# Optimization experiments

Measured on AMD Instinct MI355X. Metric: run time of the kernel, lower is better.

The kernel has to match this reference:

```python
import jax, jax.numpy as jnp
import numpy as np

B, N, D, H = 2, 2048, 2048, 16
HD = D // H  # head_dim = 128


def _rope(x, cos, sin):
    # x: [B,H,N,HD]; cos/sin: [N,HD]. use_real=True, use_real_unbind_dim=-1 (interleaved pairs).
    xr = x[..., 0::2]
    xi = x[..., 1::2]
    x_rot = jnp.stack([-xi, xr], axis=-1).reshape(x.shape)
    return x * cos[None, None] + x_rot * sin[None, None]


def setup_inputs() -> dict:
    key = jax.random.key(0)
    ks = jax.random.split(key, 10)
    x = jax.random.normal(ks[0], (B, N, D), dtype=jnp.float32)
    # realistic RoPE tables
    inv_freq = 1.0 / (10000.0 ** (np.arange(0, HD, 2, dtype=np.float32) / HD))
    t = np.arange(N, dtype=np.float32)
    ang = np.einsum('n,f->nf', t, inv_freq)           # [N, HD/2]
    ang = np.repeat(ang, 2, axis=-1)                  # [N, HD] interleaved
    cos = jnp.asarray(np.cos(ang))
    sin = jnp.asarray(np.sin(ang))
    s = 0.02
    Wq = jax.random.normal(ks[1], (D, D), dtype=jnp.float32) * s
    Wk = jax.random.normal(ks[2], (D, D), dtype=jnp.float32) * s
    Wv = jax.random.normal(ks[3], (D, D), dtype=jnp.float32) * s
    Wo = jax.random.normal(ks[4], (D, D), dtype=jnp.float32) * s
    bq = jnp.zeros((D,), jnp.float32)
    bk = jnp.zeros((D,), jnp.float32)
    bv = jnp.zeros((D,), jnp.float32)
    bo = jnp.zeros((D,), jnp.float32)
    return {"x": x, "cos": cos, "sin": sin, "Wq": Wq, "bq": bq, "Wk": Wk,
            "bk": bk, "Wv": Wv, "bv": bv, "Wo": Wo, "bo": bo}


def reference(x, cos, sin, Wq, bq, Wk, bk, Wv, bv, Wo, bo):
    scale = HD ** -0.5
    q = x @ Wq + bq
    k = x @ Wk + bk
    v = x @ Wv + bv
    # b n (h c) -> b h n c
    def split_heads(t):
        return t.reshape(B, N, H, HD).transpose(0, 2, 1, 3)
    q, k, v = split_heads(q), split_heads(k), split_heads(v)
    q = q * scale  # module's dp_scale
    q = _rope(q, cos, sin)
    k = _rope(k, cos, sin)
    # flash_attn_func(softmax_scale=None) applies head_dim^-0.5 AGAIN -> effective HD^-1
    logits = jnp.einsum('bhqc,bhkc->bhqk', q, k) * scale
    attn = jax.nn.softmax(logits, axis=-1)
    o = jnp.einsum('bhqk,bhkc->bhqc', attn, v)
    o = o.transpose(0, 2, 1, 3).reshape(B, N, D)  # b h n c -> b n (h c)
    return o @ Wo + bo
```

## Files before the change

### kernel.cpp

```cpp
#include <hip/hip_runtime.h>

typedef unsigned short u16;
typedef unsigned int u32;
typedef __attribute__((ext_vector_type(8))) short bfx8;
typedef __attribute__((ext_vector_type(4))) float fx4;
typedef __attribute__((ext_vector_type(16))) float fx16;
typedef __attribute__((ext_vector_type(4))) unsigned short u16x4;

#define MFMA_BF16(a,b,c)   __builtin_amdgcn_mfma_f32_16x16x32_bf16((a),(b),(c),0,0,0)
#define MFMA32_BF16(a,b,c) __builtin_amdgcn_mfma_f32_32x32x16_bf16((a),(b),(c),0,0,0)

#define BATCH 2
#define SEQ   2048
#define DM    2048
#define NH    16
#define HD    128
#define MR    4096

__device__ __forceinline__ u16 f2bf(float f){
  union{float f; unsigned u;} v; v.f = f;
  unsigned r = v.u + 0x7FFFu + ((v.u >> 16) & 1u);
  return (u16)(r >> 16);
}
__device__ __forceinline__ unsigned cvtpk(float lo, float hi){
  unsigned r;
  asm("v_cvt_pk_bf16_f32 %0, %1, %2" : "=v"(r) : "v"(lo), "v"(hi));
  return r;
}
__device__ __forceinline__ void gll16(const void* g, void* l){
  __builtin_amdgcn_global_load_lds(
      (const __attribute__((address_space(1))) void*)g,
      (__attribute__((address_space(3))) void*)l, 16, 0, 0);
}

__global__ __launch_bounds__(256) void k_cast(const float* __restrict__ in,
                                              u16* __restrict__ o, int n4){
  int gid = blockIdx.x*256 + threadIdx.x;
  if (gid >= n4) return;
  float4 x = ((const float4*)in)[gid];
  u16x4 v = {f2bf(x.x), f2bf(x.y), f2bf(x.z), f2bf(x.w)};
  ((u16x4*)o)[gid] = v;
}

__global__ __launch_bounds__(256) void k_twcat(const float* __restrict__ Wq,
                                               const float* __restrict__ Wk,
                                               const float* __restrict__ Wv,
                                               u16* __restrict__ Th){
  __shared__ float T[64][65];
  int z = blockIdx.z;
  const float* W = (z==0) ? Wq : (z==1) ? Wk : Wv;
  int n0 = blockIdx.x*64, k0 = blockIdx.y*64;
  int t = threadIdx.x;
  int r = t>>2, c = (t&3)*16;
  const float* src = W + (size_t)(k0+r)*DM + n0 + c;
  #pragma unroll
  for (int j=0;j<4;j++){
    float4 v = *(const float4*)(src + 4*j);
    T[r][c+4*j+0]=v.x; T[r][c+4*j+1]=v.y; T[r][c+4*j+2]=v.z; T[r][c+4*j+3]=v.w;
  }
  __syncthreads();
  int nr = t>>2, kc = (t&3)*16;
  size_t ob = (size_t)(z*DM + n0+nr)*DM + k0 + kc;
  #pragma unroll
  for (int j=0;j<16;j+=4){
    u16x4 vh;
    #pragma unroll
    for (int q=0;q<4;q++) vh[q] = f2bf(T[kc+j+q][nr]);
    *(u16x4*)(Th+ob+j)=vh;
  }
}

__global__ __launch_bounds__(256) void k_tw(const float* __restrict__ W, u16* __restrict__ Th){
  __shared__ float T[64][65];
  int n0 = blockIdx.x*64, k0 = blockIdx.y*64;
  int t = threadIdx.x;
  int r = t>>2, c = (t&3)*16;
  const float* src = W + (size_t)(k0+r)*DM + n0 + c;
  #pragma unroll
  for (int j=0;j<4;j++){
    float4 v = *(const float4*)(src + 4*j);
    T[r][c+4*j+0]=v.x; T[r][c+4*j+1]=v.y; T[r][c+4*j+2]=v.z; T[r][c+4*j+3]=v.w;
  }
  __syncthreads();
  int nr = t>>2, kc = (t&3)*16;
  size_t ob = (size_t)(n0+nr)*DM + k0 + kc;
  #pragma unroll
  for (int j=0;j<16;j+=4){
    u16x4 vh;
    #pragma unroll
    for (int q=0;q<4;q++) vh[q] = f2bf(T[kc+j+q][nr]);
    *(u16x4*)(Th+ob+j)=vh;
  }
}

__global__ __launch_bounds__(256) void k_gemm_qkv(
    const u16* __restrict__ A, const u16* __restrict__ B,
    const float* __restrict__ bqp, const float* __restrict__ bkp, const float* __restrict__ bvp,
    const float* __restrict__ cs, const float* __restrict__ sn,
    u16* __restrict__ qb, u16* __restrict__ kb, u16* __restrict__ vt)
{
  __shared__ u16 sA[128*64], sB[128*64];
  const int K = DM;
  const int tid = threadIdx.x;
  const int lane = tid & 63;
  const int w = tid >> 6;
  const int g = lane >> 4, qi = lane & 15;
  const int wr = w >> 1, wc = w & 1;
  const int bm = blockIdx.y * 128;
  const int bn = blockIdx.x * 128;

  int r_[4], sc_[4];
  #pragma unroll
  for (int i=0;i<4;i++){
    int off = w*4096 + i*1024 + lane*16;
    int r = off>>7, cb = off&127;
    r_[i] = r; sc_[i] = (cb ^ ((r&7)<<4)) >> 1;
  }

  fx4 acc[4][4] = {};

  for (int k0 = 0; k0 < K; k0 += 64){
    __syncthreads();
    #pragma unroll
    for (int i=0;i<4;i++){
      gll16(A + (size_t)(bm + r_[i])*K + k0 + sc_[i], &sA[w*2048 + i*512]);
      gll16(B + (size_t)(bn + r_[i])*K + k0 + sc_[i], &sB[w*2048 + i*512]);
    }
    __syncthreads();

    #pragma unroll
    for (int kk=0;kk<2;kk++){
      const int cb = kk*64 + g*16;
      bfx8 fa[4], fb[4];
      #pragma unroll
      for (int m=0;m<4;m++){
        int row = wr*64 + m*16 + qi;
        fa[m] = *(const bfx8*)((const char*)sA + row*128 + (cb ^ ((row&7)<<4)));
      }
      #pragma unroll
      for (int n=0;n<4;n++){
        int row = wc*64 + n*16 + qi;
        fb[n] = *(const bfx8*)((const char*)sB + row*128 + (cb ^ ((row&7)<<4)));
      }
      #pragma unroll
      for (int m=0;m<4;m++)
        #pragma unroll
        for (int n=0;n<4;n++)
          acc[m][n] = MFMA_BF16(fa[m], fb[n], acc[m][n]);
    }
  }

  const int sec = bn >> 11;
  if (sec < 2){
    u16* dst = sec ? kb : qb;
    const float* bias = sec ? bkp : bqp;
    const float qs = sec ? 1.0f : (1.4426950408889634f/128.0f);
    #pragma unroll
    for (int m=0;m<4;m++){
      #pragma unroll
      for (int n=0;n<4;n++){
        int col = bn + wc*64 + n*16 + qi;
        int cq = col & 2047, hh = cq>>7, d = cq&127;
        float bc = bias[cq];
        float sgn = (d&1) ? 1.0f : -1.0f;
        #pragma unroll
        for (int r=0;r<4;r++){
          int row = bm + wr*64 + m*16 + g*4 + r;
          int bI = row>>11, nr2 = row&2047;
          float v = (acc[m][n][r] + bc)*qs;
          float p = __shfl_xor(v, 1, 64);
          float c = cs[nr2*HD + d], s = sn[nr2*HD + d];
          float y = v*c + sgn*p*s;
          dst[((size_t)(bI*NH+hh)*SEQ + nr2)*HD + d] = f2bf(y);
        }
      }
    }
  } else {
    #pragma unroll
    for (int m=0;m<4;m++){
      #pragma unroll
      for (int n=0;n<4;n++){
        int col = bn + wc*64 + n*16 + qi;
        int cv = col & 2047, hh = cv>>7, d = cv&127;
        float bc = bvp[cv];
        int row0 = bm + wr*64 + m*16 + g*4;
        int bI = row0>>11, n0_ = row0&2047;
        u16x4 pk;
        #pragma unroll
        for (int r=0;r<4;r++) pk[r] = f2bf(acc[m][n][r] + bc);
        *(u16x4*)(vt + ((size_t)(bI*NH+hh)*HD + d)*SEQ + n0_) = pk;
      }
    }
  }
}

__global__ __launch_bounds__(256) void k_gemm(
    const u16* __restrict__ A, const u16* __restrict__ B,
    const float* __restrict__ bias, float* __restrict__ C,
    int M, int N, int K)
{
  __shared__ u16 sA[128*64], sB[128*64];
  const int tid = threadIdx.x;
  const int lane = tid & 63;
  const int w = tid >> 6;
  const int g = lane >> 4, qi = lane & 15;
  const int wr = w >> 1, wc = w & 1;
  const int bm = blockIdx.y * 128;
  const int bn = blockIdx.x * 128;

  int r_[4], sc_[4];
  #pragma unroll
  for (int i=0;i<4;i++){
    int off = w*4096 + i*1024 + lane*16;
    int r = off>>7, cb = off&127;
    r_[i] = r; sc_[i] = (cb ^ ((r&7)<<4)) >> 1;
  }

  fx4 acc[4][4] = {};

  for (int k0 = 0; k0 < K; k0 += 64){
    __syncthreads();
    #pragma unroll
    for (int i=0;i<4;i++){
      gll16(A + (size_t)(bm + r_[i])*K + k0 + sc_[i], &sA[w*2048 + i*512]);
      gll16(B + (size_t)(bn + r_[i])*K + k0 + sc_[i], &sB[w*2048 + i*512]);
    }
    __syncthreads();

    #pragma unroll
    for (int kk=0;kk<2;kk++){
      const int cb = kk*64 + g*16;
      bfx8 fa[4], fb[4];
      #pragma unroll
      for (int m=0;m<4;m++){
        int row = wr*64 + m*16 + qi;
        fa[m] = *(const bfx8*)((const char*)sA + row*128 + (cb ^ ((row&7)<<4)));
      }
      #pragma unroll
      for (int n=0;n<4;n++){
        int row = wc*64 + n*16 + qi;
        fb[n] = *(const bfx8*)((const char*)sB + row*128 + (cb ^ ((row&7)<<4)));
      }
      #pragma unroll
      for (int m=0;m<4;m++)
        #pragma unroll
        for (int n=0;n<4;n++)
          acc[m][n] = MFMA_BF16(fa[m], fb[n], acc[m][n]);
    }
  }

  #pragma unroll
  for (int m=0;m<4;m++){
    #pragma unroll
    for (int n=0;n<4;n++){
      int col = bn + wc*64 + n*16 + qi;
      float bc = bias[col];
      #pragma unroll
      for (int r=0;r<4;r++){
        int row = bm + wr*64 + m*16 + g*4 + r;
        C[(size_t)row*N + col] = acc[m][n][r] + bc;
      }
    }
  }
}

__global__ __launch_bounds__(128) void k_flash(const u16* __restrict__ Q, const u16* __restrict__ Kb,
                                               const u16* __restrict__ Vt, u16* __restrict__ O){
  __shared__ union SM {
    struct { u16 k[64*128]; u16 v[128*64]; } s;
    u16 ob[64*128];
  } sm;
  const int tid = threadIdx.x, lane = tid & 63, w = tid >> 6;
  const int bid = blockIdx.x;
  const int qt = bid & 31, h = (bid>>5)&15, b = bid>>9;
  const int bh = b*NH + h;
  const int qb0 = qt*64;
  const int hi = lane >> 5, qi = lane & 31;
  const u16* Kb2 = Kb + (size_t)bh*SEQ*HD;
  const u16* Vt2 = Vt + (size_t)bh*SEQ*HD;

  bfx8 qf[8];
  {
    const u16* qp = Q + ((size_t)bh*SEQ + qb0 + w*32 + qi)*HD + hi*8;
    #pragma unroll
    for (int ks=0; ks<8; ++ks) qf[ks] = *(const bfx8*)(qp + ks*16);
  }

  u32 koff[8], voff[8];
  #pragma unroll
  for (int i=0;i<8;i++){
    int off = w*8192 + i*1024 + lane*16;
    int kr = off>>8, kc = off&255;
    int kcs = kc ^ ((kr&15)<<4);
    koff[i] = kr*HD + (kcs>>1);
    int vr = off>>7, vc = off&127;
    int vcs = vc ^ ((vr&7)<<4);
    voff[i] = vr*SEQ + (vcs>>1);
  }

#define STAGE_K(kv_) do { _Pragma("unroll") \
    for (int i_=0;i_<8;i_++) gll16(Kb2 + koff[i_] + (u32)(kv_)*HD, &sm.s.k[w*4096 + i_*512]); } while(0)
#define STAGE_V(kv_) do { _Pragma("unroll") \
    for (int i_=0;i_<8;i_++) gll16(Vt2 + voff[i_] + (u32)(kv_),    &sm.s.v[w*4096 + i_*512]); } while(0)

  fx16 accO0 = {}, accO1 = {}, accO2 = {}, accO3 = {};
  float mrun = -1e30f, lrun = 0.f;

  STAGE_K(0);
  STAGE_V(0);

  for (int t=0; t<32; ++t){
    asm volatile("s_waitcnt vmcnt(8)" ::: "memory");
    __builtin_amdgcn_s_barrier();

    fx16 stA = {}, stB = {};
    __builtin_amdgcn_s_setprio(1);
    #pragma unroll
    for (int ks=0; ks<8; ++ks){
      const int cb = ks*32 + hi*16;
      int rowA = qi;
      int rowB = 32 + qi;
      bfx8 kfa = *(const bfx8*)((const char*)sm.s.k + rowA*256 + (cb ^ ((rowA&15)<<4)));
      bfx8 kfb = *(const bfx8*)((const char*)sm.s.k + rowB*256 + (cb ^ ((rowB&15)<<4)));
      stA = MFMA32_BF16(kfa, qf[ks], stA);
      stB = MFMA32_BF16(kfb, qf[ks], stB);
    }
    __builtin_amdgcn_s_setprio(0);
    __builtin_amdgcn_s_barrier();
    if (t < 31) STAGE_K(t*64 + 64);

    float pm = stA[0];
    #pragma unroll
    for (int i=1;i<16;i++) pm = fmaxf(pm, stA[i]);
    #pragma unroll
    for (int i=0;i<16;i++) pm = fmaxf(pm, stB[i]);
    pm = fmaxf(pm, __shfl_xor(pm, 32, 64));
    if (!__all(pm <= mrun + 11.0f)){
      float mn = fmaxf(mrun, pm);
      float al = exp2f(mrun - mn);
      lrun *= al;
      accO0 *= al; accO1 *= al; accO2 *= al; accO3 *= al;
      mrun = mn;
    }
    float ps = 0.f;
    #pragma unroll
    for (int i=0;i<16;i++){
      float p0 = exp2f(stA[i] - mrun); stA[i] = p0; ps += p0;
      float p1 = exp2f(stB[i] - mrun); stB[i] = p1; ps += p1;
    }
    lrun += ps;

    bfx8 pv0, pv1, pv2, pv3;
#define PACK(pvx_, stX_, base_) do { \
      unsigned a0 = cvtpk(stX_[base_+0], stX_[base_+1]); \
      unsigned a1 = cvtpk(stX_[base_+2], stX_[base_+3]); \
      unsigned b0 = cvtpk(stX_[base_+4], stX_[base_+5]); \
      unsigned b1 = cvtpk(stX_[base_+6], stX_[base_+7]); \
      asm volatile("v_permlane32_swap_b32 %0, %1" : "+v"(a0), "+v"(b0)); \
      asm volatile("v_permlane32_swap_b32 %0, %1" : "+v"(a1), "+v"(b1)); \
      union { bfx8 v; unsigned u[4]; } pu_; \
      pu_.u[0] = a0; pu_.u[1] = a1; pu_.u[2] = b0; pu_.u[3] = b1; \
      pvx_ = pu_.v; } while(0)
    PACK(pv0, stA, 0);
    PACK(pv1, stA, 8);
    PACK(pv2, stB, 0);
    PACK(pv3, stB, 8);
#undef PACK

    asm volatile("s_waitcnt vmcnt(8)" ::: "memory");
    if (t == 31) asm volatile("s_waitcnt vmcnt(0)" ::: "memory");
    __builtin_amdgcn_s_barrier();

    __builtin_amdgcn_s_setprio(1);
    #pragma unroll
    for (int dblk=0; dblk<4; ++dblk){
      const int row = dblk*32 + qi;
      const int swz = (row&7)<<4;
      const char* vrow = (const char*)sm.s.v + row*128;
      bfx8 vf0 = *(const bfx8*)(vrow + ((0*32 + hi*16) ^ swz));
      bfx8 vf1 = *(const bfx8*)(vrow + ((1*32 + hi*16) ^ swz));
      bfx8 vf2 = *(const bfx8*)(vrow + ((2*32 + hi*16) ^ swz));
      bfx8 vf3 = *(const bfx8*)(vrow + ((3*32 + hi*16) ^ swz));
      fx16 a = (dblk==0)?accO0:(dblk==1)?accO1:(dblk==2)?accO2:accO3;
      a = MFMA32_BF16(vf0, pv0, a);
      a = MFMA32_BF16(vf1, pv1, a);
      a = MFMA32_BF16(vf2, pv2, a);
      a = MFMA32_BF16(vf3, pv3, a);
      if (dblk==0) accO0 = a; else if (dblk==1) accO1 = a; else if (dblk==2) accO2 = a; else accO3 = a;
    }
    __builtin_amdgcn_s_setprio(0);
    __builtin_amdgcn_s_barrier();
    if (t < 31) STAGE_V(t*64 + 64);
  }
#undef STAGE_K
#undef STAGE_V

  {
    float l = lrun + __shfl_xor(lrun, 32, 64);
    float inv = 1.0f / l;
    int q = w*32 + qi;
    char* obr = (char*)sm.ob + q*256;
    const int swz = (q&7)<<4;
#define OWRITE(accX_, dblk_) do { _Pragma("unroll") \
    for (int p=0;p<8;p++){ \
      int d = dblk_*32 + 2*(p&1) + 8*(p>>1) + 4*hi; \
      unsigned wv = cvtpk(accX_[2*p]*inv, accX_[2*p+1]*inv); \
      *(unsigned*)(obr + ((d*2) ^ swz)) = wv; } } while(0)
    OWRITE(accO0, 0); OWRITE(accO1, 1); OWRITE(accO2, 2); OWRITE(accO3, 3);
#undef OWRITE
  }
  __syncthreads();
  {
    int q2 = tid>>1, c0 = (tid&1)*64;
    u16* dst = O + (size_t)(b*SEQ + qb0 + q2)*DM + h*HD + c0;
    #pragma unroll
    for (int jj=0;jj<8;jj++){
      int d0 = c0 + jj*8;
      bfx8 v = *(const bfx8*)((const char*)sm.ob + q2*256 + ((d0*2) ^ ((q2&7)<<4)));
      *(bfx8*)(dst + jj*8) = v;
    }
  }
}

extern "C" void kernel_launch(void* const* d_in, const int* in_sizes, int n_in,
                              void* d_out, int out_size, void* d_ws, size_t ws_size,
                              hipStream_t stream){
  (void)in_sizes; (void)n_in; (void)out_size; (void)ws_size;
  const float* x  = (const float*)d_in[0];
  const float* cs = (const float*)d_in[1];
  const float* sn = (const float*)d_in[2];
  const float* Wq = (const float*)d_in[3];
  const float* bq = (const float*)d_in[4];
  const float* Wk = (const float*)d_in[5];
  const float* bk = (const float*)d_in[6];
  const float* Wv = (const float*)d_in[7];
  const float* bv = (const float*)d_in[8];
  const float* Wo = (const float*)d_in[9];
  const float* bo = (const float*)d_in[10];
  float* out = (float*)d_out;

  char* ws = (char*)d_ws;
  const size_t MB = 1048576;
  u16* xb   = (u16*)(ws);
  u16* wt   = (u16*)(ws + 16*MB);
  u16* qb   = (u16*)(ws + 40*MB);
  u16* kb   = (u16*)(ws + 56*MB);
  u16* vt   = (u16*)(ws + 72*MB);
  u16* ob16 = (u16*)(ws + 88*MB);

  k_cast<<<8192,256,0,stream>>>(x, xb, 2097152);
  k_twcat<<<dim3(32,32,3),256,0,stream>>>(Wq, Wk, Wv, wt);
  k_gemm_qkv<<<dim3(48,32),256,0,stream>>>(xb, wt, bq, bk, bv, cs, sn, qb, kb, vt);

  k_flash<<<1024,128,0,stream>>>(qb, kb, vt, ob16);

  k_tw<<<dim3(32,32),256,0,stream>>>(Wo, wt);
  k_gemm<<<dim3(16,32),256,0,stream>>>(ob16, wt, bo, out, MR, DM, DM);
}
```

Measured before the change: 328.4 us.

## Enlarge QKV GEMM tile to 256x256 with double-buffered LDS and XCD-aware block swizzle

```diff
diff --git a/kernel.cpp b/kernel.cpp
--- a/kernel.cpp
+++ b/kernel.cpp
@@ -93,62 +93,90 @@
   }
 }
 
-__global__ __launch_bounds__(256) void k_gemm_qkv(
+__global__ __launch_bounds__(512,2) void k_gemm_qkv(
     const u16* __restrict__ A, const u16* __restrict__ B,
     const float* __restrict__ bqp, const float* __restrict__ bkp, const float* __restrict__ bvp,
     const float* __restrict__ cs, const float* __restrict__ sn,
     u16* __restrict__ qb, u16* __restrict__ kb, u16* __restrict__ vt)
 {
-  __shared__ u16 sA[128*64], sB[128*64];
+  __shared__ u16 sA[2][256*64], sB[2][256*64];
   const int K = DM;
   const int tid = threadIdx.x;
   const int lane = tid & 63;
   const int w = tid >> 6;
   const int g = lane >> 4, qi = lane & 15;
-  const int wr = w >> 1, wc = w & 1;
-  const int bm = blockIdx.y * 128;
-  const int bn = blockIdx.x * 128;
-
-  int r_[4], sc_[4];
+  const int wr = w >> 2, wc = w & 3;
+  const int bid = blockIdx.x;
+  const int sid = (bid & 7)*48 + (bid >> 3);
+  const int bx = sid % 24, by = sid / 24;
+  const int bm = by*256, bn = bx*256;
+
+  u32 r_[4], c_[4];
   #pragma unroll
   for (int i=0;i<4;i++){
-    int off = w*4096 + i*1024 + lane*16;
+    int off = i*8192 + w*1024 + lane*16;
     int r = off>>7, cb = off&127;
-    r_[i] = r; sc_[i] = (cb ^ ((r&7)<<4)) >> 1;
-  }
-
-  fx4 acc[4][4] = {};
-
-  for (int k0 = 0; k0 < K; k0 += 64){
-    __syncthreads();
-    #pragma unroll
-    for (int i=0;i<4;i++){
-      gll16(A + (size_t)(bm + r_[i])*K + k0 + sc_[i], &sA[w*2048 + i*512]);
-      gll16(B + (size_t)(bn + r_[i])*K + k0 + sc_[i], &sB[w*2048 + i*512]);
-    }
-    __syncthreads();
-
-    #pragma unroll
-    for (int kk=0;kk<2;kk++){
-      const int cb = kk*64 + g*16;
-      bfx8 fa[4], fb[4];
-      #pragma unroll
-      for (int m=0;m<4;m++){
-        int row = wr*64 + m*16 + qi;
-        fa[m] = *(const bfx8*)((const char*)sA + row*128 + (cb ^ ((row&7)<<4)));
-      }
-      #pragma unroll
-      for (int n=0;n<4;n++){
-        int row = wc*64 + n*16 + qi;
-        fb[n] = *(const bfx8*)((const char*)sB + row*128 + (cb ^ ((row&7)<<4)));
-      }
-      #pragma unroll
-      for (int m=0;m<4;m++)
+    r_[i] = r; c_[i] = (u32)((cb ^ ((r&7)<<4)) >> 1);
+  }
+  const u16* Aw = A + (size_t)bm*K;
+  const u16* Bw = B + (size_t)bn*K;
+
+#define STAGE(s_, k0_) do { _Pragma("unroll") \
+  for (int i_=0;i_<4;i_++){ \
+    gll16(Aw + (size_t)r_[i_]*K + (k0_) + c_[i_], &sA[s_][i_*4096 + w*512]); \
+    gll16(Bw + (size_t)r_[i_]*K + (k0_) + c_[i_], &sB[s_][i_*4096 + w*512]); } } while(0)
+
+  fx4 acc[8][4] = {};
+
+  STAGE(0, 0);
+  int cur = 0;
+  for (int kt = 0; kt < 32; ++kt){
+    if (kt < 31){
+      STAGE(cur^1, (kt+1)*64);
+      asm volatile("s_waitcnt vmcnt(8)" ::: "memory");
+    } else {
+      asm volatile("s_waitcnt vmcnt(0)" ::: "memory");
+    }
+    __builtin_amdgcn_s_barrier();
+
+    const char* a0 = (const char*)sA[cur];
+    const char* b0 = (const char*)sB[cur];
+    bfx8 fb[4][2];
+    #pragma unroll
+    for (int n=0;n<4;n++){
+      int row = wc*64 + n*16 + qi;
+      #pragma unroll
+      for (int kk=0;kk<2;kk++){
+        int cb2 = kk*64 + g*16;
+        fb[n][kk] = *(const bfx8*)(b0 + row*128 + (cb2 ^ ((row&7)<<4)));
+      }
+    }
+    #pragma unroll
+    for (int p=0;p<4;p++){
+      bfx8 fa[2][2];
+      #pragma unroll
+      for (int mm=0;mm<2;mm++){
+        int row = wr*128 + (p*2+mm)*16 + qi;
+        #pragma unroll
+        for (int kk=0;kk<2;kk++){
+          int cb2 = kk*64 + g*16;
+          fa[mm][kk] = *(const bfx8*)(a0 + row*128 + (cb2 ^ ((row&7)<<4)));
+        }
+      }
+      __builtin_amdgcn_s_setprio(1);
+      #pragma unroll
+      for (int mm=0;mm<2;mm++)
         #pragma unroll
         for (int n=0;n<4;n++)
-          acc[m][n] = MFMA_BF16(fa[m], fb[n], acc[m][n]);
-    }
-  }
+          #pragma unroll
+          for (int kk=0;kk<2;kk++)
+            acc[p*2+mm][n] = MFMA_BF16(fa[mm][kk], fb[n][kk], acc[p*2+mm][n]);
+      __builtin_amdgcn_s_setprio(0);
+    }
+    __builtin_amdgcn_s_barrier();
+    cur ^= 1;
+  }
+#undef STAGE
 
   const int sec = bn >> 11;
   if (sec < 2){
@@ -156,7 +184,7 @@
     const float* bias = sec ? bkp : bqp;
     const float qs = sec ? 1.0f : (1.4426950408889634f/128.0f);
     #pragma unroll
-    for (int m=0;m<4;m++){
+    for (int m=0;m<8;m++){
       #pragma unroll
       for (int n=0;n<4;n++){
         int col = bn + wc*64 + n*16 + qi;
@@ -165,7 +193,7 @@
         float sgn = (d&1) ? 1.0f : -1.0f;
         #pragma unroll
         for (int r=0;r<4;r++){
-          int row = bm + wr*64 + m*16 + g*4 + r;
+          int row = bm + wr*128 + m*16 + g*4 + r;
           int bI = row>>11, nr2 = row&2047;
           float v = (acc[m][n][r] + bc)*qs;
           float p = __shfl_xor(v, 1, 64);
@@ -177,13 +205,13 @@
     }
   } else {
     #pragma unroll
-    for (int m=0;m<4;m++){
+    for (int m=0;m<8;m++){
       #pragma unroll
       for (int n=0;n<4;n++){
         int col = bn + wc*64 + n*16 + qi;
         int cv = col & 2047, hh = cv>>7, d = cv&127;
         float bc = bvp[cv];
-        int row0 = bm + wr*64 + m*16 + g*4;
+        int row0 = bm + wr*128 + m*16 + g*4;
         int bI = row0>>11, n0_ = row0&2047;
         u16x4 pk;
         #pragma unroll
@@ -271,7 +299,8 @@
     u16 ob[64*128];
   } sm;
   const int tid = threadIdx.x, lane = tid & 63, w = tid >> 6;
-  const int bid = blockIdx.x;
+  const int bid0 = blockIdx.x;
+  const int bid = ((bid0 & 7) << 7) | (bid0 >> 3);
   const int qt = bid & 31, h = (bid>>5)&15, b = bid>>9;
   const int bh = b*NH + h;
   const int qb0 = qt*64;
@@ -450,7 +479,7 @@
 
   k_cast<<<8192,256,0,stream>>>(x, xb, 2097152);
   k_twcat<<<dim3(32,32,3),256,0,stream>>>(Wq, Wk, Wv, wt);
-  k_gemm_qkv<<<dim3(48,32),256,0,stream>>>(xb, wt, bq, bk, bv, cs, sn, qb, kb, vt);
+  k_gemm_qkv<<<384,512,0,stream>>>(xb, wt, bq, bk, bv, cs, sn, qb, kb, vt);
 
   k_flash<<<1024,128,0,stream>>>(qb, kb, vt, ob16);
 
```

Result: slower. 339.1 us (+3.2%).
